# Optimization experiments

Hardware: AMD Instinct MI355X
Metric: run time of the kernel (lower is better)

The kernel has to match this reference:

```python
import jax, jax.numpy as jnp
import numpy as np
from jax import lax

SR = 44100  # sample_rate from __init__ default


def _log_scale(v, mn, mx):
    # Faithful to AudioParameter.validate_and_scale with scale='log':
    # clamp, map log(v) to [0,1] over [log(mn), log(mx)], then rescale LINEARLY to [mn, mx].
    v = float(np.clip(float(v), mn, mx))
    log_min = np.log(max(mn, 1e-6))
    log_max = np.log(mx)
    normalized = (np.log(max(v, 1e-6)) - log_min) / (log_max - log_min)
    return normalized * (mx - mn) + mn


def _eq_coeffs(frequency, gain, q, sr=SR):
    # Parameter validation/scaling (frequency, q are 'log' scale; gain is linear clamp)
    f = _log_scale(frequency, 20.0, 20000.0)
    g = float(np.clip(float(gain), -30.0, 30.0))
    Q = _log_scale(q, 0.1, 30.0)
    # torchaudio.functional.equalizer_biquad ('bell' peaking EQ) coefficients
    w0 = 2.0 * np.pi * f / sr
    A = 10.0 ** (g / 40.0)
    alpha = np.sin(w0) / (2.0 * Q)
    b0 = 1.0 + alpha * A
    b1 = -2.0 * np.cos(w0)
    b2 = 1.0 - alpha * A
    a0 = 1.0 + alpha / A
    a1 = b1
    a2 = 1.0 - alpha / A
    return (b0 / a0, b1 / a0, b2 / a0, a1 / a0, a2 / a0)


def _biquad(x, coefs):
    # Direct-form-I second-order IIR along last axis, vectorized over all leading dims.
    b0, b1, b2, a1, a2 = [jnp.asarray(c, x.dtype) for c in coefs]
    shp = x.shape
    xf = x.reshape(-1, shp[-1])  # (N, T)
    z = jnp.zeros((xf.shape[0],), x.dtype)

    def step(carry, xn):
        x1, x2, y1, y2 = carry
        yn = b0 * xn + b1 * x1 + b2 * x2 - a1 * y1 - a2 * y2
        return (xn, x1, yn, y1), yn

    _, ys = lax.scan(step, (z, z, z, z), xf.T)  # ys: (T, N)
    return ys.T.reshape(shp)


def setup_inputs() -> dict:
    key = jax.random.key(0)
    audio = jax.random.normal(key, (32, 2, 441000), dtype=jnp.float32)  # 10s stereo, batch 32
    return {"audio": audio, "frequency": 2000, "gain": 6, "q": 1}


def reference(audio, frequency, gain, q):
    # filter_type='bell' (default) -> torchaudio equalizer_biquad path
    coefs = _eq_coeffs(frequency, gain, q)
    return _biquad(audio, coefs)
```

## Files before the change

kernel.cpp:

```cpp
#include <hip/hip_runtime.h>
#include <math.h>

#ifndef M_PI
#define M_PI 3.14159265358979323846
#endif

#define T_LEN      441000
#define L          16
#define TILE       (64 * L)
#define WARM       256
#define WARM_LN    (WARM / L)
#define CHAIN_OUT  (2 * TILE - WARM)
#define WPC        ((T_LEN + CHAIN_OUT - 1) / CHAIN_OUT)
#define BLOCK      256
#define BLK_X      ((WPC + 3) / 4)


__device__ __forceinline__ double log_scale(double v, double mn, double mx) {
    v = fmin(fmax(v, mn), mx);
    double lmin = log(fmax(mn, 1e-6));
    double lmax = log(mx);
    double nrm = (log(fmax(v, 1e-6)) - lmin) / (lmax - lmin);
    return nrm * (mx - mn) + mn;
}

__global__ void eq_setup_kernel(const int* __restrict__ f_in,
                                const int* __restrict__ g_in,
                                const int* __restrict__ q_in,
                                float* __restrict__ ws) {
    double f = log_scale((double)f_in[0], 20.0, 20000.0);
    double g = fmin(fmax((double)g_in[0], -30.0), 30.0);
    double Q = log_scale((double)q_in[0], 0.1, 30.0);
    double w0 = 2.0 * M_PI * f / 44100.0;
    double A  = pow(10.0, g / 40.0);
    double al = sin(w0) / (2.0 * Q);
    double ca = cos(w0);
    double b0 = 1.0 + al * A;
    double b1 = -2.0 * ca;
    double b2 = 1.0 - al * A;
    double a0 = 1.0 + al / A;
    double B0 = b0 / a0, B1 = b1 / a0, B2 = b2 / a0;
    double A1 = b1 / a0, A2 = (1.0 - al / A) / a0;
    ws[0] = (float)B0; ws[1] = (float)B1; ws[2] = (float)B2;
    ws[3] = (float)A1; ws[4] = (float)A2;

    const double m11 = -A1, m12 = -A2;

    double p11 = m11, p12 = m12, p21 = 1.0, p22 = 0.0;
    for (int i = 0; i < 4; ++i) {
        double s11 = p11 * p11 + p12 * p21;
        double s12 = p11 * p12 + p12 * p22;
        double s21 = p21 * p11 + p22 * p21;
        double s22 = p21 * p12 + p22 * p22;
        p11 = s11; p12 = s12; p21 = s21; p22 = s22;
    }
    for (int j = 0; j < 6; ++j) {
        ws[5 + 4 * j + 0] = (float)p11;
        ws[5 + 4 * j + 1] = (float)p12;
        ws[5 + 4 * j + 2] = (float)p21;
        ws[5 + 4 * j + 3] = (float)p22;
        double s11 = p11 * p11 + p12 * p21;
        double s12 = p11 * p12 + p12 * p22;
        double s21 = p21 * p11 + p22 * p21;
        double s22 = p21 * p12 + p22 * p22;
        p11 = s11; p12 = s12; p21 = s21; p22 = s22;
    }

    double q11 = m11, q12 = m12, q21 = 1.0, q22 = 0.0;
    for (int k = 0; k < L; ++k) {
        ws[29 + 2 * k] = (float)q11;
        ws[30 + 2 * k] = (float)q12;
        const double n11 = m11 * q11 + m12 * q21;
        const double n12 = m11 * q12 + m12 * q22;
        q21 = q11; q22 = q12;
        q11 = n11; q12 = n12;
    }
}

__device__ __forceinline__ void load_tile(const float* __restrict__ xc, int base,
                                          float4& vm, float4& v0, float4& v1,
                                          float4& v2, float4& v3) {
    if (base >= 4 && base + L <= T_LEN) {
        vm = *reinterpret_cast<const float4*>(xc + base - 4);
        v0 = *reinterpret_cast<const float4*>(xc + base + 0);
        v1 = *reinterpret_cast<const float4*>(xc + base + 4);
        v2 = *reinterpret_cast<const float4*>(xc + base + 8);
        v3 = *reinterpret_cast<const float4*>(xc + base + 12);
    } else {
        float e[20];
#pragma unroll
        for (int k = 0; k < 20; ++k) {
            const int idx = base - 4 + k;
            e[k] = (idx >= 0 && idx < T_LEN) ? xc[idx] : 0.f;
        }
        vm = make_float4(e[0],  e[1],  e[2],  e[3]);
        v0 = make_float4(e[4],  e[5],  e[6],  e[7]);
        v1 = make_float4(e[8],  e[9],  e[10], e[11]);
        v2 = make_float4(e[12], e[13], e[14], e[15]);
        v3 = make_float4(e[16], e[17], e[18], e[19]);
    }
}

__device__ __forceinline__ void tile_pass(const float* __restrict__ ws, int lane,
        float4 vm, float4 v0, float4 v1, float4 v2, float4 v3,
        bool first, float& g0, float& g1,
        float* __restrict__ yc, int base, bool gate) {
    const float b0 = ws[0], b1 = ws[1], b2 = ws[2], a1 = ws[3], a2 = ws[4];

    float xv[L];
    xv[0]=v0.x;  xv[1]=v0.y;  xv[2]=v0.z;  xv[3]=v0.w;
    xv[4]=v1.x;  xv[5]=v1.y;  xv[6]=v1.z;  xv[7]=v1.w;
    xv[8]=v2.x;  xv[9]=v2.y;  xv[10]=v2.z; xv[11]=v2.w;
    xv[12]=v3.x; xv[13]=v3.y; xv[14]=v3.z; xv[15]=v3.w;
    const float xm2 = vm.z, xm1 = vm.w;

    float yl[L];
    float c0 = 0.f, c1 = 0.f;
    {
        float xk1 = xm1, xk2 = xm2;
#pragma unroll
        for (int k = 0; k < L; ++k) {
            const float xk = xv[k];
            const float t  = fmaf(b0, xk, fmaf(b1, xk1, b2 * xk2));
            const float yn = fmaf(-a1, c0, fmaf(-a2, c1, t));
            c1 = c0; c0 = yn;
            xk2 = xk1; xk1 = xk;
            yl[k] = yn;
        }
    }

    if (!first && lane == 0) {
        const float n0 = fmaf(ws[5], g0, fmaf(ws[6], g1, c0));
        const float n1 = fmaf(ws[7], g0, fmaf(ws[8], g1, c1));
        c0 = n0; c1 = n1;
    }

#pragma unroll
    for (int j = 0; j < 6; ++j) {
        const float m11 = ws[5 + 4 * j + 0], m12 = ws[5 + 4 * j + 1];
        const float m21 = ws[5 + 4 * j + 2], m22 = ws[5 + 4 * j + 3];
        const float d0 = __shfl_up(c0, 1u << j);
        const float d1 = __shfl_up(c1, 1u << j);
        if (lane >= (1 << j)) {
            c0 = fmaf(m11, d0, fmaf(m12, d1, c0));
            c1 = fmaf(m21, d0, fmaf(m22, d1, c1));
        }
    }

    const float ng0 = __shfl(c0, 63), ng1 = __shfl(c1, 63);
    float s0 = __shfl_up(c0, 1);
    float s1 = __shfl_up(c1, 1);
    if (lane == 0) { s0 = first ? 0.f : g0; s1 = first ? 0.f : g1; }
    g0 = ng0; g1 = ng1;

    if (gate && base < T_LEN) {
        if (base + L <= T_LEN) {
#pragma unroll
            for (int q = 0; q < L / 4; ++q) {
                float o[4];
#pragma unroll
                for (int r = 0; r < 4; ++r) {
                    const int k = 4 * q + r;
                    o[r] = fmaf(ws[29 + 2 * k], s0, fmaf(ws[30 + 2 * k], s1, yl[k]));
                }
                *reinterpret_cast<float4*>(yc + base + 4 * q) =
                    make_float4(o[0], o[1], o[2], o[3]);
            }
        } else {
#pragma unroll
            for (int k = 0; k < L; ++k)
                if (base + k < T_LEN)
                    yc[base + k] = fmaf(ws[29 + 2 * k], s0, fmaf(ws[30 + 2 * k], s1, yl[k]));
        }
    }
}

__global__ __launch_bounds__(BLOCK, 4) void eq_main_kernel(
        const float* __restrict__ x,
        const float* __restrict__ ws,
        float* __restrict__ y) {
    const int tid   = threadIdx.x;
    const int lane  = tid & 63;
    const int wv    = tid >> 6;
    const int chain = blockIdx.x * (BLOCK / 64) + wv;
    if (chain >= WPC) return;
    const int ch = blockIdx.y;

    const float* __restrict__ xc = x + (size_t)ch * T_LEN;
    float*       __restrict__ yc = y + (size_t)ch * T_LEN;

    const int base0 = chain * CHAIN_OUT - WARM + lane * L;
    const int base1 = base0 + TILE;

    float4 Am, A0, A1, A2, A3, Bm, B0, B1, B2, B3;
    load_tile(xc, base0, Am, A0, A1, A2, A3);
    load_tile(xc, base1, Bm, B0, B1, B2, B3);

    float g0 = 0.f, g1 = 0.f;
    tile_pass(ws, lane, Am, A0, A1, A2, A3, true,  g0, g1, yc, base0, lane >= WARM_LN);
    tile_pass(ws, lane, Bm, B0, B1, B2, B3, false, g0, g1, yc, base1, true);
}

extern "C" void kernel_launch(void* const* d_in, const int* in_sizes, int n_in,
                              void* d_out, int out_size, void* d_ws, size_t ws_size,
                              hipStream_t stream) {
    const float* x = (const float*)d_in[0];
    const int*   f = (const int*)d_in[1];
    const int*   g = (const int*)d_in[2];
    const int*   q = (const int*)d_in[3];
    float*       y  = (float*)d_out;
    float*       ws = (float*)d_ws;

    eq_setup_kernel<<<1, 1, 0, stream>>>(f, g, q, ws);

    const int nch = in_sizes[0] / T_LEN;
    dim3 grid(BLK_X, nch);
    eq_main_kernel<<<grid, dim3(BLOCK), 0, stream>>>(x, ws, y);
}
```

Measured before the change: 217.0 us.

## Use persistent grid-stride waves with double-buffered tile prefetch

Each wave now processes a single 1024-sample tile per chain, with the first 16 lanes acting as warm-up, instead of two chained tiles. A fixed grid of 1024 blocks walks the chains grid-stride style and prefetches the next tile's inputs into registers while the current tile is filtered, with sched_barriers keeping the load ahead of the compute. The intent is to overlap global-memory latency with the scan arithmetic and cut launch and tail overhead. In exchange the warm-up overhead grows, since a quarter of each wave's loads and compute are spent on overlap, and register pressure rises from double buffering.

```diff
diff --git a/kernel.cpp b/kernel.cpp
--- a/kernel.cpp
+++ b/kernel.cpp
@@ -7,13 +7,11 @@
 
 #define T_LEN      441000
 #define L          16
-#define TILE       (64 * L)
-#define WARM       256
-#define WARM_LN    (WARM / L)
-#define CHAIN_OUT  (2 * TILE - WARM)
-#define WPC        ((T_LEN + CHAIN_OUT - 1) / CHAIN_OUT)
+#define WARM_LN    16
+#define OUT_W      ((64 - WARM_LN) * L)
+#define WPC        ((T_LEN + OUT_W - 1) / OUT_W)
 #define BLOCK      256
-#define BLK_X      ((WPC + 3) / 4)
+#define NBLK       1024
 
 
 __device__ __forceinline__ double log_scale(double v, double mn, double mx) {
@@ -77,9 +75,13 @@
     }
 }
 
-__device__ __forceinline__ void load_tile(const float* __restrict__ xc, int base,
-                                          float4& vm, float4& v0, float4& v1,
-                                          float4& v2, float4& v3) {
+__device__ __forceinline__ void load_chain(const float* __restrict__ x, int c, int lane,
+                                           float4& vm, float4& v0, float4& v1,
+                                           float4& v2, float4& v3) {
+    const int ch   = c / WPC;
+    const int pos  = c - ch * WPC;
+    const int base = pos * OUT_W - WARM_LN * L + lane * L;
+    const float* __restrict__ xc = x + (size_t)ch * T_LEN;
     if (base >= 4 && base + L <= T_LEN) {
         vm = *reinterpret_cast<const float4*>(xc + base - 4);
         v0 = *reinterpret_cast<const float4*>(xc + base + 0);
@@ -101,10 +103,14 @@
     }
 }
 
-__device__ __forceinline__ void tile_pass(const float* __restrict__ ws, int lane,
+__device__ __forceinline__ void tile_pass(const float* __restrict__ ws, int lane, int c,
         float4 vm, float4 v0, float4 v1, float4 v2, float4 v3,
-        bool first, float& g0, float& g1,
-        float* __restrict__ yc, int base, bool gate) {
+        float* __restrict__ y) {
+    const int ch   = c / WPC;
+    const int pos  = c - ch * WPC;
+    const int base = pos * OUT_W - WARM_LN * L + lane * L;
+    float* __restrict__ yc = y + (size_t)ch * T_LEN;
+
     const float b0 = ws[0], b1 = ws[1], b2 = ws[2], a1 = ws[3], a2 = ws[4];
 
     float xv[L];
@@ -127,12 +133,6 @@
             xk2 = xk1; xk1 = xk;
             yl[k] = yn;
         }
-    }
-
-    if (!first && lane == 0) {
-        const float n0 = fmaf(ws[5], g0, fmaf(ws[6], g1, c0));
-        const float n1 = fmaf(ws[7], g0, fmaf(ws[8], g1, c1));
-        c0 = n0; c1 = n1;
     }
 
 #pragma unroll
@@ -147,13 +147,11 @@
         }
     }
 
-    const float ng0 = __shfl(c0, 63), ng1 = __shfl(c1, 63);
     float s0 = __shfl_up(c0, 1);
     float s1 = __shfl_up(c1, 1);
-    if (lane == 0) { s0 = first ? 0.f : g0; s1 = first ? 0.f : g1; }
-    g0 = ng0; g1 = ng1;
-
-    if (gate && base < T_LEN) {
+    if (lane == 0) { s0 = 0.f; s1 = 0.f; }
+
+    if (lane >= WARM_LN && base < T_LEN) {
         if (base + L <= T_LEN) {
 #pragma unroll
             for (int q = 0; q < L / 4; ++q) {
@@ -178,27 +176,35 @@
 __global__ __launch_bounds__(BLOCK, 4) void eq_main_kernel(
         const float* __restrict__ x,
         const float* __restrict__ ws,
-        float* __restrict__ y) {
-    const int tid   = threadIdx.x;
-    const int lane  = tid & 63;
-    const int wv    = tid >> 6;
-    const int chain = blockIdx.x * (BLOCK / 64) + wv;
-    if (chain >= WPC) return;
-    const int ch = blockIdx.y;
-
-    const float* __restrict__ xc = x + (size_t)ch * T_LEN;
-    float*       __restrict__ yc = y + (size_t)ch * T_LEN;
-
-    const int base0 = chain * CHAIN_OUT - WARM + lane * L;
-    const int base1 = base0 + TILE;
+        float* __restrict__ y,
+        int ntot) {
+    const int lane    = threadIdx.x & 63;
+    const int wid     = blockIdx.x * (BLOCK / 64) + (threadIdx.x >> 6);
+    const int wstride = gridDim.x * (BLOCK / 64);
+
+    int c = wid;
+    if (c >= ntot) return;
 
     float4 Am, A0, A1, A2, A3, Bm, B0, B1, B2, B3;
-    load_tile(xc, base0, Am, A0, A1, A2, A3);
-    load_tile(xc, base1, Bm, B0, B1, B2, B3);
-
-    float g0 = 0.f, g1 = 0.f;
-    tile_pass(ws, lane, Am, A0, A1, A2, A3, true,  g0, g1, yc, base0, lane >= WARM_LN);
-    tile_pass(ws, lane, Bm, B0, B1, B2, B3, false, g0, g1, yc, base1, true);
+    load_chain(x, c, lane, Am, A0, A1, A2, A3);
+
+    for (;;) {
+        const int cn = c + wstride;
+        const bool hn = (cn < ntot);
+        if (hn) load_chain(x, cn, lane, Bm, B0, B1, B2, B3);
+        __builtin_amdgcn_sched_barrier(0);
+        tile_pass(ws, lane, c, Am, A0, A1, A2, A3, y);
+        if (!hn) break;
+        c = cn;
+
+        const int cn2 = c + wstride;
+        const bool hn2 = (cn2 < ntot);
+        if (hn2) load_chain(x, cn2, lane, Am, A0, A1, A2, A3);
+        __builtin_amdgcn_sched_barrier(0);
+        tile_pass(ws, lane, c, Bm, B0, B1, B2, B3, y);
+        if (!hn2) break;
+        c = cn2;
+    }
 }
 
 extern "C" void kernel_launch(void* const* d_in, const int* in_sizes, int n_in,
@@ -213,7 +219,7 @@
 
     eq_setup_kernel<<<1, 1, 0, stream>>>(f, g, q, ws);
 
-    const int nch = in_sizes[0] / T_LEN;
-    dim3 grid(BLK_X, nch);
-    eq_main_kernel<<<grid, dim3(BLOCK), 0, stream>>>(x, ws, y);
-}
+    const int nch  = in_sizes[0] / T_LEN;
+    const int ntot = nch * WPC;
+    eq_main_kernel<<<dim3(NBLK), dim3(BLOCK), 0, stream>>>(x, ws, y, ntot);
+}
```

After: 222.3 us. 1.02x slower.
